# Kernel tuning notes

Hardware: AMD Instinct MI355X
Metric: run time of the kernel (lower is better)

## Reference

```python
import jax, jax.numpy as jnp
import numpy as np

EPS = 1e-06
SINKHORN_ITERS = 3


def _sinkhorn_knopp(P, iters=SINKHORN_ITERS, eps=EPS):
    # P: [n, n] positive matrix -> approximately doubly stochastic
    for _ in range(iters):
        P = P / (P.sum(axis=-1, keepdims=True) + eps)
        P = P / (P.sum(axis=-2, keepdims=True) + eps)
    return P


def setup_inputs() -> dict:
    key = jax.random.key(0)
    k1, k2, k3, k4 = jax.random.split(key, 4)
    B, n, C = 8192, 4, 2048
    x = jax.random.normal(k1, (B, n, C), dtype=jnp.float32)
    rmsnorm_weight = jnp.ones((C,), dtype=jnp.float32)
    H_pre = jax.random.normal(k2, (n,), dtype=jnp.float32)
    H_post = jax.random.normal(k3, (n,), dtype=jnp.float32)
    H_res = jax.random.normal(k4, (n, n), dtype=jnp.float32)
    return {"x": x, "rmsnorm_weight": rmsnorm_weight, "H_pre": H_pre,
            "H_post": H_post, "H_res": H_res}


def reference(x, rmsnorm_weight, H_pre, H_post, H_res):
    # x: [B, n, C] float32
    # 1) sigmoid-weighted stream aggregation: [B, C]
    H_pre_act = jax.nn.sigmoid(H_pre)
    x_agg = jnp.einsum('bnc,n->bc', x, H_pre_act)
    # 2) RMSNorm in bf16 (rms computed in fp32, matching torch fallback)
    x_agg_bf16 = x_agg.astype(jnp.bfloat16)
    rms = jnp.sqrt(jnp.mean(x_agg_bf16.astype(jnp.float32) ** 2, axis=-1,
                            keepdims=True) + EPS)  # [B, 1] fp32
    w_bf16 = rmsnorm_weight.astype(jnp.bfloat16)
    y_norm = x_agg_bf16 / rms * w_bf16[None, :]  # promoted to fp32 by rms
    # 3) Sinkhorn-Knopp on exp(H_res): [n, n]
    M = _sinkhorn_knopp(jnp.exp(H_res))
    # 4) mix streams and combine
    H_post_act = 2.0 * jax.nn.sigmoid(H_post)
    mixed = jnp.einsum('ij,bjc->bic', M, x)  # [B, n, C]
    out = mixed + H_post_act[None, :, None] * y_norm.astype(jnp.float32)[:, None, :]
    return out
```

## Files before the change

kernel.cpp:

```cpp
#include <hip/hip_runtime.h>
#include <hip/hip_bf16.h>


namespace {

constexpr int N = 4;
constexpr int C = 2048;
constexpr int BLOCK = 256;
constexpr int CPT = C / BLOCK;
constexpr int VEC = CPT / 4;
constexpr int BPB = 4;
constexpr float EPSF = 1e-6f;

typedef float f4 __attribute__((ext_vector_type(4)));

__device__ __forceinline__ float bf16r(float v) {
    return __bfloat162float(__float2bfloat16(v));
}

__global__ void setup_kernel(const float* __restrict__ H_pre,
                             const float* __restrict__ H_post,
                             const float* __restrict__ H_res,
                             float* __restrict__ cst) {
    if (threadIdx.x != 0 || blockIdx.x != 0) return;
    float P[N][N];
    #pragma unroll
    for (int j = 0; j < N; ++j) {
        cst[j]     = 1.0f / (1.0f + expf(-H_pre[j]));
        cst[N + j] = 2.0f / (1.0f + expf(-H_post[j]));
    }
    #pragma unroll
    for (int i = 0; i < N; ++i)
        #pragma unroll
        for (int j = 0; j < N; ++j)
            P[i][j] = expf(H_res[i * N + j]);
    #pragma unroll
    for (int it = 0; it < 3; ++it) {
        #pragma unroll
        for (int i = 0; i < N; ++i) {
            float rs = P[i][0] + P[i][1] + P[i][2] + P[i][3] + EPSF;
            #pragma unroll
            for (int j = 0; j < N; ++j) P[i][j] /= rs;
        }
        #pragma unroll
        for (int j = 0; j < N; ++j) {
            float cs = P[0][j] + P[1][j] + P[2][j] + P[3][j] + EPSF;
            #pragma unroll
            for (int i = 0; i < N; ++i) P[i][j] /= cs;
        }
    }
    #pragma unroll
    for (int i = 0; i < N; ++i)
        #pragma unroll
        for (int j = 0; j < N; ++j)
            cst[2 * N + i * N + j] = P[i][j];
}

__device__ __forceinline__ void load_x(const float* __restrict__ x,
                                       size_t base, int t,
                                       float (&xs)[N][CPT]) {
    #pragma unroll
    for (int j = 0; j < N; ++j) {
        #pragma unroll
        for (int v = 0; v < VEC; ++v) {
            const f4 tmp = __builtin_nontemporal_load(
                (const f4*)(x + base + (size_t)j * C + (size_t)(v * BLOCK + t) * 4));
            #pragma unroll
            for (int k = 0; k < 4; ++k) xs[j][v * 4 + k] = tmp[k];
        }
    }
}

__device__ __forceinline__ void process_b(const float (&xs)[N][CPT],
                                          const float (&ws)[CPT],
                                          const float (&pre)[N],
                                          const float (&post)[N],
                                          const float (&M)[N][N],
                                          float (&sr)[BLOCK / 64],
                                          int t, size_t base,
                                          float* __restrict__ out) {
    float agg[CPT];
    float ss = 0.0f;
    #pragma unroll
    for (int k = 0; k < CPT; ++k) {
        float a = pre[0] * xs[0][k] + pre[1] * xs[1][k]
                + pre[2] * xs[2][k] + pre[3] * xs[3][k];
        a = bf16r(a);
        agg[k] = a;
        ss += a * a;
    }

    #pragma unroll
    for (int off = 32; off > 0; off >>= 1) ss += __shfl_xor(ss, off, 64);
    if ((t & 63) == 0) sr[t >> 6] = ss;
    __syncthreads();
    float tot = 0.0f;
    #pragma unroll
    for (int i = 0; i < BLOCK / 64; ++i) tot += sr[i];
    const float rinv = 1.0f / sqrtf(tot * (1.0f / (float)C) + EPSF);

    float yn[CPT];
    #pragma unroll
    for (int k = 0; k < CPT; ++k) yn[k] = agg[k] * rinv * ws[k];

    #pragma unroll
    for (int i = 0; i < N; ++i) {
        #pragma unroll
        for (int v = 0; v < VEC; ++v) {
            f4 o;
            #pragma unroll
            for (int k = 0; k < 4; ++k) {
                const int idx = v * 4 + k;
                o[k] = M[i][0] * xs[0][idx] + M[i][1] * xs[1][idx]
                     + M[i][2] * xs[2][idx] + M[i][3] * xs[3][idx]
                     + post[i] * yn[idx];
            }
            __builtin_nontemporal_store(
                o, (f4*)(out + base + (size_t)i * C + (size_t)(v * BLOCK + t) * 4));
        }
    }
}

__global__ __launch_bounds__(BLOCK) void mhc_kernel(
    const float* __restrict__ x,
    const float* __restrict__ w,
    const float* __restrict__ cst,
    float* __restrict__ out,
    int B)
{
    const int t = threadIdx.x;
    const int b0 = blockIdx.x * BPB;
    if (b0 >= B) return;
    const int nb = (B - b0 < BPB) ? (B - b0) : BPB;

    __shared__ float s_red[2][BLOCK / 64];

    float pre[N], post[N], M[N][N];
    #pragma unroll
    for (int j = 0; j < N; ++j) {
        pre[j]  = cst[j];
        post[j] = cst[N + j];
    }
    #pragma unroll
    for (int i = 0; i < N; ++i)
        #pragma unroll
        for (int j = 0; j < N; ++j)
            M[i][j] = cst[2 * N + i * N + j];

    float ws[CPT];
    #pragma unroll
    for (int v = 0; v < VEC; ++v) {
        const f4 tmp = *(const f4*)(w + (size_t)(v * BLOCK + t) * 4);
        #pragma unroll
        for (int k = 0; k < 4; ++k) ws[v * 4 + k] = bf16r(tmp[k]);
    }

    const size_t row = (size_t)N * C;
    float xsA[N][CPT], xsB[N][CPT];

    load_x(x, (size_t)b0 * row, t, xsA);

    if (nb > 1) load_x(x, (size_t)(b0 + 1) * row, t, xsB);
    process_b(xsA, ws, pre, post, M, s_red[0], t, (size_t)b0 * row, out);

    if (nb > 1) {
        if (nb > 2) load_x(x, (size_t)(b0 + 2) * row, t, xsA);
        process_b(xsB, ws, pre, post, M, s_red[1], t, (size_t)(b0 + 1) * row, out);
    }
    if (nb > 2) {
        if (nb > 3) load_x(x, (size_t)(b0 + 3) * row, t, xsB);
        process_b(xsA, ws, pre, post, M, s_red[0], t, (size_t)(b0 + 2) * row, out);
    }
    if (nb > 3) {
        process_b(xsB, ws, pre, post, M, s_red[1], t, (size_t)(b0 + 3) * row, out);
    }
}

}

extern "C" void kernel_launch(void* const* d_in, const int* in_sizes, int n_in,
                              void* d_out, int out_size, void* d_ws, size_t ws_size,
                              hipStream_t stream) {
    const float* x      = (const float*)d_in[0];
    const float* w      = (const float*)d_in[1];
    const float* H_pre  = (const float*)d_in[2];
    const float* H_post = (const float*)d_in[3];
    const float* H_res  = (const float*)d_in[4];
    float* out = (float*)d_out;
    float* cst = (float*)d_ws;

    const int B = in_sizes[0] / (N * C);

    setup_kernel<<<dim3(1), dim3(1), 0, stream>>>(H_pre, H_post, H_res, cst);

    const int grid = (B + BPB - 1) / BPB;
    mhc_kernel<<<dim3(grid), dim3(BLOCK), 0, stream>>>(x, w, cst, out, B);
}
```

Measured before the change: 433.7 us.

## Map one batch row per wavefront and fold setup into the main kernel

Each 64-lane wavefront now owns a whole batch row (128 floats per lane), so the RMS reduction needs only intra-wave shuffles, and the shared-memory barrier goes away. The separate single-thread setup kernel is removed: every wave recomputes the sigmoids and the Sinkhorn normalisation redundantly and broadcasts them via readfirstlane. The intent is to save the extra launch and the block-level sync. In exchange, register pressure per lane is much higher (512 x values), software double-buffering across rows is dropped, and the hint of 2 blocks per SIMD may cause spills.

```diff
diff --git a/kernel.cpp b/kernel.cpp
--- a/kernel.cpp
+++ b/kernel.cpp
@@ -7,9 +7,9 @@
 constexpr int N = 4;
 constexpr int C = 2048;
 constexpr int BLOCK = 256;
-constexpr int CPT = C / BLOCK;
-constexpr int VEC = CPT / 4;
-constexpr int BPB = 4;
+constexpr int WPB = BLOCK / 64;
+constexpr int CPL = C / 64;
+constexpr int VEC = CPL / 4;
 constexpr float EPSF = 1e-6f;
 
 typedef float f4 __attribute__((ext_vector_type(4)));
@@ -17,17 +17,47 @@
 __device__ __forceinline__ float bf16r(float v) {
     return __bfloat162float(__float2bfloat16(v));
 }
+__device__ __forceinline__ float rfl(float v) {
+    return __uint_as_float(__builtin_amdgcn_readfirstlane(__float_as_uint(v)));
+}
 
-__global__ void setup_kernel(const float* __restrict__ H_pre,
-                             const float* __restrict__ H_post,
-                             const float* __restrict__ H_res,
-                             float* __restrict__ cst) {
-    if (threadIdx.x != 0 || blockIdx.x != 0) return;
-    float P[N][N];
+__global__ __launch_bounds__(BLOCK, 2) void mhc_kernel(
+    const float* __restrict__ x,
+    const float* __restrict__ w,
+    const float* __restrict__ H_pre,
+    const float* __restrict__ H_post,
+    const float* __restrict__ H_res,
+    float* __restrict__ out,
+    int B)
+{
+    const int lane = threadIdx.x & 63;
+    const int wv   = threadIdx.x >> 6;
+    const int b    = blockIdx.x * WPB + wv;
+    if (b >= B) return;
+
+    f4 wraw[VEC];
+    #pragma unroll
+    for (int v = 0; v < VEC; ++v)
+        wraw[v] = *(const f4*)(w + (size_t)(v * 64 + lane) * 4);
+
+    const size_t base = (size_t)b * (N * C);
+    float xs[N][CPL];
     #pragma unroll
     for (int j = 0; j < N; ++j) {
-        cst[j]     = 1.0f / (1.0f + expf(-H_pre[j]));
-        cst[N + j] = 2.0f / (1.0f + expf(-H_post[j]));
+        #pragma unroll
+        for (int v = 0; v < VEC; ++v) {
+            const f4 tmp = __builtin_nontemporal_load(
+                (const f4*)(x + base + (size_t)j * C + (size_t)(v * 64 + lane) * 4));
+            #pragma unroll
+            for (int k = 0; k < 4; ++k) xs[j][v * 4 + k] = tmp[k];
+        }
+    }
+
+    float pre[N], post[N], P[N][N];
+    #pragma unroll
+    for (int j = 0; j < N; ++j) {
+        pre[j]  = 1.0f / (1.0f + expf(-H_pre[j]));
+        post[j] = 2.0f / (1.0f + expf(-H_post[j]));
     }
     #pragma unroll
     for (int i = 0; i < N; ++i)
@@ -38,51 +68,29 @@
     for (int it = 0; it < 3; ++it) {
         #pragma unroll
         for (int i = 0; i < N; ++i) {
-            float rs = P[i][0] + P[i][1] + P[i][2] + P[i][3] + EPSF;
+            const float rs = P[i][0] + P[i][1] + P[i][2] + P[i][3] + EPSF;
             #pragma unroll
             for (int j = 0; j < N; ++j) P[i][j] /= rs;
         }
         #pragma unroll
         for (int j = 0; j < N; ++j) {
-            float cs = P[0][j] + P[1][j] + P[2][j] + P[3][j] + EPSF;
+            const float cs = P[0][j] + P[1][j] + P[2][j] + P[3][j] + EPSF;
             #pragma unroll
             for (int i = 0; i < N; ++i) P[i][j] /= cs;
         }
     }
     #pragma unroll
+    for (int j = 0; j < N; ++j) { pre[j] = rfl(pre[j]); post[j] = rfl(post[j]); }
+    #pragma unroll
     for (int i = 0; i < N; ++i)
         #pragma unroll
         for (int j = 0; j < N; ++j)
-            cst[2 * N + i * N + j] = P[i][j];
-}
+            P[i][j] = rfl(P[i][j]);
 
-__device__ __forceinline__ void load_x(const float* __restrict__ x,
-                                       size_t base, int t,
-                                       float (&xs)[N][CPT]) {
-    #pragma unroll
-    for (int j = 0; j < N; ++j) {
-        #pragma unroll
-        for (int v = 0; v < VEC; ++v) {
-            const f4 tmp = __builtin_nontemporal_load(
-                (const f4*)(x + base + (size_t)j * C + (size_t)(v * BLOCK + t) * 4));
-            #pragma unroll
-            for (int k = 0; k < 4; ++k) xs[j][v * 4 + k] = tmp[k];
-        }
-    }
-}
-
-__device__ __forceinline__ void process_b(const float (&xs)[N][CPT],
-                                          const float (&ws)[CPT],
-                                          const float (&pre)[N],
-                                          const float (&post)[N],
-                                          const float (&M)[N][N],
-                                          float (&sr)[BLOCK / 64],
-                                          int t, size_t base,
-                                          float* __restrict__ out) {
-    float agg[CPT];
+    float agg[CPL];
     float ss = 0.0f;
     #pragma unroll
-    for (int k = 0; k < CPT; ++k) {
+    for (int k = 0; k < CPL; ++k) {
         float a = pre[0] * xs[0][k] + pre[1] * xs[1][k]
                 + pre[2] * xs[2][k] + pre[3] * xs[3][k];
         a = bf16r(a);
@@ -92,16 +100,14 @@
 
     #pragma unroll
     for (int off = 32; off > 0; off >>= 1) ss += __shfl_xor(ss, off, 64);
-    if ((t & 63) == 0) sr[t >> 6] = ss;
-    __syncthreads();
-    float tot = 0.0f;
+    const float rinv = 1.0f / sqrtf(ss * (1.0f / (float)C) + EPSF);
+
+    float yn[CPL];
     #pragma unroll
-    for (int i = 0; i < BLOCK / 64; ++i) tot += sr[i];
-    const float rinv = 1.0f / sqrtf(tot * (1.0f / (float)C) + EPSF);
-
-    float yn[CPT];
-    #pragma unroll
-    for (int k = 0; k < CPT; ++k) yn[k] = agg[k] * rinv * ws[k];
+    for (int v = 0; v < VEC; ++v)
+        #pragma unroll
+        for (int k = 0; k < 4; ++k)
+            yn[v * 4 + k] = agg[v * 4 + k] * rinv * bf16r(wraw[v][k]);
 
     #pragma unroll
     for (int i = 0; i < N; ++i) {
@@ -109,70 +115,15 @@
         for (int v = 0; v < VEC; ++v) {
             f4 o;
             #pragma unroll
-            for (int k = 0; k < 4; ++k) {
-                const int idx = v * 4 + k;
-                o[k] = M[i][0] * xs[0][idx] + M[i][1] * xs[1][idx]
-                     + M[i][2] * xs[2][idx] + M[i][3] * xs[3][idx]
-                     + post[i] * yn[idx];
+            for (int k4 = 0; k4 < 4; ++k4) {
+                const int idx = v * 4 + k4;
+                o[k4] = P[i][0] * xs[0][idx] + P[i][1] * xs[1][idx]
+                      + P[i][2] * xs[2][idx] + P[i][3] * xs[3][idx]
+                      + post[i] * yn[idx];
             }
             __builtin_nontemporal_store(
-                o, (f4*)(out + base + (size_t)i * C + (size_t)(v * BLOCK + t) * 4));
+                o, (f4*)(out + base + (size_t)i * C + (size_t)(v * 64 + lane) * 4));
         }
-    }
-}
-
-__global__ __launch_bounds__(BLOCK) void mhc_kernel(
-    const float* __restrict__ x,
-    const float* __restrict__ w,
-    const float* __restrict__ cst,
-    float* __restrict__ out,
-    int B)
-{
-    const int t = threadIdx.x;
-    const int b0 = blockIdx.x * BPB;
-    if (b0 >= B) return;
-    const int nb = (B - b0 < BPB) ? (B - b0) : BPB;
-
-    __shared__ float s_red[2][BLOCK / 64];
-
-    float pre[N], post[N], M[N][N];
-    #pragma unroll
-    for (int j = 0; j < N; ++j) {
-        pre[j]  = cst[j];
-        post[j] = cst[N + j];
-    }
-    #pragma unroll
-    for (int i = 0; i < N; ++i)
-        #pragma unroll
-        for (int j = 0; j < N; ++j)
-            M[i][j] = cst[2 * N + i * N + j];
-
-    float ws[CPT];
-    #pragma unroll
-    for (int v = 0; v < VEC; ++v) {
-        const f4 tmp = *(const f4*)(w + (size_t)(v * BLOCK + t) * 4);
-        #pragma unroll
-        for (int k = 0; k < 4; ++k) ws[v * 4 + k] = bf16r(tmp[k]);
-    }
-
-    const size_t row = (size_t)N * C;
-    float xsA[N][CPT], xsB[N][CPT];
-
-    load_x(x, (size_t)b0 * row, t, xsA);
-
-    if (nb > 1) load_x(x, (size_t)(b0 + 1) * row, t, xsB);
-    process_b(xsA, ws, pre, post, M, s_red[0], t, (size_t)b0 * row, out);
-
-    if (nb > 1) {
-        if (nb > 2) load_x(x, (size_t)(b0 + 2) * row, t, xsA);
-        process_b(xsB, ws, pre, post, M, s_red[1], t, (size_t)(b0 + 1) * row, out);
-    }
-    if (nb > 2) {
-        if (nb > 3) load_x(x, (size_t)(b0 + 3) * row, t, xsB);
-        process_b(xsA, ws, pre, post, M, s_red[0], t, (size_t)(b0 + 2) * row, out);
-    }
-    if (nb > 3) {
-        process_b(xsB, ws, pre, post, M, s_red[1], t, (size_t)(b0 + 3) * row, out);
     }
 }
 
@@ -187,12 +138,11 @@
     const float* H_post = (const float*)d_in[3];
     const float* H_res  = (const float*)d_in[4];
     float* out = (float*)d_out;
-    float* cst = (float*)d_ws;
+    (void)d_ws; (void)ws_size;
 
     const int B = in_sizes[0] / (N * C);
 
-    setup_kernel<<<dim3(1), dim3(1), 0, stream>>>(H_pre, H_post, H_res, cst);
-
-    const int grid = (B + BPB - 1) / BPB;
-    mhc_kernel<<<dim3(grid), dim3(BLOCK), 0, stream>>>(x, w, cst, out, B);
+    const int grid = (B + WPB - 1) / WPB;
+    mhc_kernel<<<dim3(grid), dim3(BLOCK), 0, stream>>>(
+        x, w, H_pre, H_post, H_res, out, B);
 }
```

Result: no change. 432.6 us (-0.3%).
